# Kernel tuning notes

Measured on AMD Instinct MI355X. Metric: run time of the kernel, lower is better.

The kernel has to match this reference:

```python
import jax, jax.numpy as jnp
import numpy as np

DIM = 256
N_HEADS = 4
B, N = 2, 4096


def setup_inputs() -> dict:
    key = jax.random.key(0)
    ks = jax.random.split(key, 10)
    s = DIM ** -0.5
    return {
        "x": jax.random.normal(ks[0], (B, N, DIM), dtype=jnp.float32),
        "q_w": jax.random.normal(ks[1], (DIM, DIM), dtype=jnp.float32) * s,
        "q_b": jnp.zeros((DIM,), dtype=jnp.float32),
        "k_w": jax.random.normal(ks[2], (DIM, DIM), dtype=jnp.float32) * s,
        "k_b": jnp.zeros((DIM,), dtype=jnp.float32),
        "v_w": jax.random.normal(ks[3], (DIM, DIM), dtype=jnp.float32) * s,
        "v_b": jnp.zeros((DIM,), dtype=jnp.float32),
        "o_w": jax.random.normal(ks[4], (DIM, DIM), dtype=jnp.float32) * s,
        "o_b": jnp.zeros((DIM,), dtype=jnp.float32),
        "tau": jnp.ones((1,), dtype=jnp.float32),
    }


def reference(x, q_w, q_b, k_w, k_b, v_w, v_b, o_w, o_b, tau):
    Bsz, Nlen, C = x.shape
    H = N_HEADS
    Dh = C // H
    scale = C ** -0.5  # source uses full dim, not head_dim
    Q = (x @ q_w.T + q_b).reshape(Bsz, Nlen, H, Dh)
    K = (x @ k_w.T + k_b).reshape(Bsz, Nlen, H, Dh)
    V = (x @ v_w.T + v_b).reshape(Bsz, Nlen, H, Dh)
    attn = jnp.einsum('bnhd,bmhd->bhnm', Q, K) * scale
    # soft-threshold gate: keep only |attn| > tau, then relu
    attn = jax.nn.relu(jnp.where(jnp.abs(attn) > tau, attn, 0.0))
    attn = jax.nn.softmax(attn, axis=-1)
    out = jnp.einsum('bhnm,bmhd->bnhd', attn, V).reshape(Bsz, Nlen, C)
    return out @ o_w.T + o_b
```

## Files before the change

kernel.cpp:

```cpp
#include <hip/hip_runtime.h>

#define SEQ   4096
#define CDIM  256
#define NHEAD 4
#define DHEAD 64
#define PSTRIDE 72
#define NSPLIT 8
#define LOG2E 1.44269504f

typedef float    f32x4 __attribute__((ext_vector_type(4)));
typedef _Float16 f16x8 __attribute__((ext_vector_type(8)));
typedef _Float16 f16x4 __attribute__((ext_vector_type(4)));

__device__ __forceinline__ f16x8 cvt_frag(const float* __restrict__ p) {
    float4 f0 = *(const float4*)p;
    float4 f1 = *(const float4*)(p + 4);
    f16x8 r;
    r[0]=(_Float16)f0.x; r[1]=(_Float16)f0.y; r[2]=(_Float16)f0.z; r[3]=(_Float16)f0.w;
    r[4]=(_Float16)f1.x; r[5]=(_Float16)f1.y; r[6]=(_Float16)f1.z; r[7]=(_Float16)f1.w;
    return r;
}

__global__ __launch_bounds__(256) void sta_prep(
    const float* __restrict__ qw, const float* __restrict__ kw,
    const float* __restrict__ vw, const float* __restrict__ ow,
    _Float16* __restrict__ w16, float* __restrict__ lfull)
{
    const int mat = blockIdx.y;
    const float* src = (mat == 0) ? qw : (mat == 1) ? kw : (mat == 2) ? vw : ow;
    const int i = (blockIdx.x * 256 + threadIdx.x) * 8;
    *(f16x8*)(w16 + mat * 65536 + i) = cvt_frag(src + i);
    const int tid = (blockIdx.y * 32 + blockIdx.x) * 256 + threadIdx.x;
    lfull[tid] = 0.0f;
}

__global__ __launch_bounds__(256) void sta_qkv(
    const float* __restrict__ x, const _Float16* __restrict__ w16,
    const float* __restrict__ qb, const float* __restrict__ kb, const float* __restrict__ vb,
    _Float16* __restrict__ Qo, _Float16* __restrict__ Ko, _Float16* __restrict__ Vo)
{
    const int wave = threadIdx.x >> 6;
    const int lane = threadIdx.x & 63;
    const int l15  = lane & 15;
    const int quad = lane >> 4;
    const int mat  = blockIdx.y;
    const int half = blockIdx.z;
    const int row0 = blockIdx.x * 64 + wave * 16;

    const _Float16* w    = w16 + mat * 65536;
    const float*    bias = (mat == 0) ? qb : (mat == 1) ? kb : vb;

    f16x8 xf[8];
    const float* xrow = x + (row0 + l15) * CDIM + quad * 8;
    #pragma unroll
    for (int ks = 0; ks < 8; ks++) xf[ks] = cvt_frag(xrow + ks * 32);

    #pragma unroll 1
    for (int ct = 0; ct < 8; ct++) {
        const int ctg = half * 8 + ct;
        const _Float16* wr = w + (ctg * 16 + l15) * CDIM + quad * 8;
        f32x4 acc = {0.f, 0.f, 0.f, 0.f};
        if (mat < 2) {
            #pragma unroll
            for (int ks = 0; ks < 8; ks++)
                acc = __builtin_amdgcn_mfma_f32_16x16x32_f16(*(const f16x8*)(wr + ks * 32), xf[ks], acc, 0, 0, 0);
            const float4 bv = *(const float4*)(bias + ctg * 16 + quad * 4);
            const int c0 = ctg * 16 + quad * 4;
            const int h = c0 >> 6, d0 = c0 & 63;
            const int grow = row0 + l15, b = grow >> 12, n = grow & (SEQ - 1);
            const float sc = (mat == 0) ? (0.0625f * LOG2E) : 1.0f;
            f16x4 o;
            o[0] = (_Float16)((acc[0] + bv.x) * sc);
            o[1] = (_Float16)((acc[1] + bv.y) * sc);
            o[2] = (_Float16)((acc[2] + bv.z) * sc);
            o[3] = (_Float16)((acc[3] + bv.w) * sc);
            _Float16* dst = ((mat == 0) ? Qo : Ko) + (((b * NHEAD + h) * SEQ + n) * DHEAD + d0);
            *(f16x4*)dst = o;
        } else {
            #pragma unroll
            for (int ks = 0; ks < 8; ks++)
                acc = __builtin_amdgcn_mfma_f32_16x16x32_f16(xf[ks], *(const f16x8*)(wr + ks * 32), acc, 0, 0, 0);
            const int c = ctg * 16 + l15;
            const int h = c >> 6, d = c & 63;
            const float bv = bias[c];
            const int grow0 = row0 + quad * 4, b = grow0 >> 12, n0 = grow0 & (SEQ - 1);
            f16x4 o;
            #pragma unroll
            for (int r = 0; r < 4; r++) o[r] = (_Float16)(acc[r] + bv);
            *(f16x4*)(Vo + (((b * NHEAD + h) * DHEAD + d) * SEQ + n0)) = o;
        }
    }
}

__global__ __launch_bounds__(256) void sta_attn(
    const _Float16* __restrict__ Q, const _Float16* __restrict__ K, const _Float16* __restrict__ Vt,
    const float* __restrict__ taup,
    _Float16* __restrict__ Opart, float* __restrict__ lfull)
{
    __shared__ __align__(16) _Float16 pbuf_all[4][64 * PSTRIDE];

    const int wave = threadIdx.x >> 6;
    const int lane = threadIdx.x & 63;
    const int l15  = lane & 15;
    const int quad = lane >> 4;
    const int qt = blockIdx.x * 4 + wave;
    const int bh = blockIdx.y;
    const int sp = blockIdx.z;
    const float tau_eff = fmaxf(taup[0], 0.0f) * LOG2E;

    const _Float16* Qb = Q  + bh * SEQ * DHEAD;
    const _Float16* Kb = K  + bh * SEQ * DHEAD;
    const _Float16* Vb = Vt + bh * DHEAD * SEQ;

    const int q0 = qt * 64;
    _Float16* pbuf = pbuf_all[wave];

    f16x8 qf[4][2];
    #pragma unroll
    for (int qb = 0; qb < 4; qb++)
        #pragma unroll
        for (int ks = 0; ks < 2; ks++)
            qf[qb][ks] = *(const f16x8*)(Qb + (q0 + qb * 16 + l15) * DHEAD + ks * 32 + quad * 8);

    f32x4 O[4][4];
    #pragma unroll
    for (int qb = 0; qb < 4; qb++)
        #pragma unroll
        for (int db = 0; db < 4; db++) O[qb][db] = (f32x4){0.f, 0.f, 0.f, 0.f};
    float rs[4] = {0.f, 0.f, 0.f, 0.f};

    #pragma unroll 1
    for (int kt = sp * 8; kt < sp * 8 + 8; kt++) {
        const int kv0 = kt * 64;

        #pragma unroll
        for (int kb = 0; kb < 4; kb++) {
            const _Float16* kp = Kb + (kv0 + kb * 16 + l15) * DHEAD + quad * 8;
            f16x8 k0 = *(const f16x8*)kp;
            f16x8 k1 = *(const f16x8*)(kp + 32);
            #pragma unroll
            for (int qb = 0; qb < 4; qb++) {
                f32x4 a = {0.f, 0.f, 0.f, 0.f};
                a = __builtin_amdgcn_mfma_f32_16x16x32_f16(k0, qf[qb][0], a, 0, 0, 0);
                a = __builtin_amdgcn_mfma_f32_16x16x32_f16(k1, qf[qb][1], a, 0, 0, 0);
                f16x4 pk;
                float acc = 0.f;
                #pragma unroll
                for (int r = 0; r < 4; r++) {
                    float e = exp2f(a[r]);
                    float p = (a[r] > tau_eff) ? e : 1.0f;
                    acc += p;
                    pk[r] = (_Float16)p;
                }
                rs[qb] += acc;
                *(f16x4*)(pbuf + (qb * 16 + l15) * PSTRIDE + kb * 16 + quad * 4) = pk;
            }
        }

        #pragma unroll
        for (int ks = 0; ks < 2; ks++) {
            f16x8 pb[4];
            #pragma unroll
            for (int qb = 0; qb < 4; qb++)
                pb[qb] = *(const f16x8*)(pbuf + (qb * 16 + l15) * PSTRIDE + ks * 32 + quad * 8);
            #pragma unroll
            for (int db = 0; db < 4; db++) {
                f16x8 vf = *(const f16x8*)(Vb + (db * 16 + l15) * SEQ + kv0 + ks * 32 + quad * 8);
                #pragma unroll
                for (int qb = 0; qb < 4; qb++)
                    O[qb][db] = __builtin_amdgcn_mfma_f32_16x16x32_f16(vf, pb[qb], O[qb][db], 0, 0, 0);
            }
        }
    }

    #pragma unroll
    for (int qb = 0; qb < 4; qb++) {
        float v = rs[qb];
        v += __shfl_xor(v, 16);
        v += __shfl_xor(v, 32);
        rs[qb] = v;
    }
    _Float16* Ob = Opart + (size_t)((sp * 8 + bh) * SEQ + q0) * DHEAD;
    #pragma unroll
    for (int qb = 0; qb < 4; qb++) {
        #pragma unroll
        for (int db = 0; db < 4; db++) {
            f16x4 ov;
            #pragma unroll
            for (int r = 0; r < 4; r++) ov[r] = (_Float16)O[qb][db][r];
            *(f16x4*)(Ob + (qb * 16 + l15) * DHEAD + db * 16 + quad * 4) = ov;
        }
    }
    if (quad == 0) {
        #pragma unroll
        for (int qb = 0; qb < 4; qb++)
            atomicAdd(&lfull[bh * SEQ + q0 + qb * 16 + l15], rs[qb]);
    }
}

__global__ __launch_bounds__(128) void sta_oproj(
    const _Float16* __restrict__ Opart, const float* __restrict__ lfull,
    const _Float16* __restrict__ w16o, const float* __restrict__ ob,
    float* __restrict__ out)
{
    const int wave = threadIdx.x >> 6;
    const int lane = threadIdx.x & 63;
    const int l15  = lane & 15;
    const int quad = lane >> 4;
    const int row0 = blockIdx.x * 32 + wave * 16;
    const int quarter = blockIdx.y;

    const int grow = row0 + l15;
    const int b = grow >> 12, n = grow & (SEQ - 1);

    _Float16 inv[NHEAD];
    #pragma unroll
    for (int h = 0; h < NHEAD; h++)
        inv[h] = (_Float16)(1.0f / lfull[(b * NHEAD + h) * SEQ + n]);

    f16x8 af[8];
    #pragma unroll
    for (int ks = 0; ks < 8; ks++) {
        const int hq = ks * 4 + quad;
        const int h  = hq >> 3;
        const int d0 = (hq & 7) * 8;
        const _Float16* pp = Opart + (size_t)((b * NHEAD + h) * SEQ + n) * DHEAD + d0;
        f16x8 s = *(const f16x8*)pp;
        #pragma unroll
        for (int sp = 1; sp < NSPLIT; sp++)
            s = s + *(const f16x8*)(pp + (size_t)sp * 8 * SEQ * DHEAD);
        af[ks] = s * inv[h];
    }

    #pragma unroll 1
    for (int ct = 0; ct < 4; ct++) {
        const int ctg = quarter * 4 + ct;
        const _Float16* wr = w16o + (ctg * 16 + l15) * CDIM + quad * 8;
        f32x4 acc = {0.f, 0.f, 0.f, 0.f};
        #pragma unroll
        for (int ks = 0; ks < 8; ks++)
            acc = __builtin_amdgcn_mfma_f32_16x16x32_f16(*(const f16x8*)(wr + ks * 32), af[ks], acc, 0, 0, 0);
        const float4 bv = *(const float4*)(ob + ctg * 16 + quad * 4);
        const int c0 = ctg * 16 + quad * 4;
        float4 res;
        res.x = acc[0] + bv.x; res.y = acc[1] + bv.y;
        res.z = acc[2] + bv.z; res.w = acc[3] + bv.w;
        *(float4*)(out + (size_t)grow * CDIM + c0) = res;
    }
}

extern "C" void kernel_launch(void* const* d_in, const int* in_sizes, int n_in,
                              void* d_out, int out_size, void* d_ws, size_t ws_size,
                              hipStream_t stream) {
    const float* x   = (const float*)d_in[0];
    const float* qw  = (const float*)d_in[1];
    const float* qb  = (const float*)d_in[2];
    const float* kw  = (const float*)d_in[3];
    const float* kb  = (const float*)d_in[4];
    const float* vw  = (const float*)d_in[5];
    const float* vb  = (const float*)d_in[6];
    const float* ow  = (const float*)d_in[7];
    const float* ob  = (const float*)d_in[8];
    const float* tau = (const float*)d_in[9];

    _Float16* w16 = (_Float16*)d_ws;
    _Float16* Q   = w16 + 262144;
    _Float16* K   = Q + 2097152;
    _Float16* Vt  = K + 2097152;
    _Float16* Opart = Vt + 2097152;
    float* lfull  = (float*)(Opart + 16777216);

    sta_prep <<<dim3(32, 4),     256, 0, stream>>>(qw, kw, vw, ow, w16, lfull);
    sta_qkv  <<<dim3(128, 3, 2), 256, 0, stream>>>(x, w16, qb, kb, vb, Q, K, Vt);
    sta_attn <<<dim3(16, 8, 8),  256, 0, stream>>>(Q, K, Vt, tau, Opart, lfull);
    sta_oproj<<<dim3(256, 4),    128, 0, stream>>>(Opart, lfull, w16 + 3 * 65536, ob, (float*)d_out);
}
```

Measured before the change: 227.5 us.

## Drop weight prep kernel, double-buffer attention tiles, replace atomics with partial sums

The separate weight-conversion kernel goes away, so the QKV and output projections read fp32 weights and convert them to fp16 inline. The QKV grid loses its column-half split, so each block now covers all 16 column tiles. The attention kernel software-pipelines K loads and QK/exp against the PV step using two LDS P buffers, and asks for 2 blocks per SM via launch bounds. Row sums are stored per split and reduced in oproj instead of atomically added, which removes the zero-init. The cost is repeated fp32 weight reads and conversions, plus higher register and LDS pressure in attention.

```diff
diff --git a/kernel.cpp b/kernel.cpp
--- a/kernel.cpp
+++ b/kernel.cpp
@@ -21,22 +21,11 @@
     return r;
 }
 
-__global__ __launch_bounds__(256) void sta_prep(
-    const float* __restrict__ qw, const float* __restrict__ kw,
-    const float* __restrict__ vw, const float* __restrict__ ow,
-    _Float16* __restrict__ w16, float* __restrict__ lfull)
-{
-    const int mat = blockIdx.y;
-    const float* src = (mat == 0) ? qw : (mat == 1) ? kw : (mat == 2) ? vw : ow;
-    const int i = (blockIdx.x * 256 + threadIdx.x) * 8;
-    *(f16x8*)(w16 + mat * 65536 + i) = cvt_frag(src + i);
-    const int tid = (blockIdx.y * 32 + blockIdx.x) * 256 + threadIdx.x;
-    lfull[tid] = 0.0f;
-}
-
 __global__ __launch_bounds__(256) void sta_qkv(
-    const float* __restrict__ x, const _Float16* __restrict__ w16,
-    const float* __restrict__ qb, const float* __restrict__ kb, const float* __restrict__ vb,
+    const float* __restrict__ x,
+    const float* __restrict__ qw, const float* __restrict__ qb,
+    const float* __restrict__ kw, const float* __restrict__ kb,
+    const float* __restrict__ vw, const float* __restrict__ vb,
     _Float16* __restrict__ Qo, _Float16* __restrict__ Ko, _Float16* __restrict__ Vo)
 {
     const int wave = threadIdx.x >> 6;
@@ -44,11 +33,10 @@
     const int l15  = lane & 15;
     const int quad = lane >> 4;
     const int mat  = blockIdx.y;
-    const int half = blockIdx.z;
     const int row0 = blockIdx.x * 64 + wave * 16;
 
-    const _Float16* w    = w16 + mat * 65536;
-    const float*    bias = (mat == 0) ? qb : (mat == 1) ? kb : vb;
+    const float* w    = (mat == 0) ? qw : (mat == 1) ? kw : vw;
+    const float* bias = (mat == 0) ? qb : (mat == 1) ? kb : vb;
 
     f16x8 xf[8];
     const float* xrow = x + (row0 + l15) * CDIM + quad * 8;
@@ -56,16 +44,15 @@
     for (int ks = 0; ks < 8; ks++) xf[ks] = cvt_frag(xrow + ks * 32);
 
     #pragma unroll 1
-    for (int ct = 0; ct < 8; ct++) {
-        const int ctg = half * 8 + ct;
-        const _Float16* wr = w + (ctg * 16 + l15) * CDIM + quad * 8;
+    for (int ct = 0; ct < 16; ct++) {
+        const float* wr = w + (ct * 16 + l15) * CDIM + quad * 8;
         f32x4 acc = {0.f, 0.f, 0.f, 0.f};
         if (mat < 2) {
             #pragma unroll
             for (int ks = 0; ks < 8; ks++)
-                acc = __builtin_amdgcn_mfma_f32_16x16x32_f16(*(const f16x8*)(wr + ks * 32), xf[ks], acc, 0, 0, 0);
-            const float4 bv = *(const float4*)(bias + ctg * 16 + quad * 4);
-            const int c0 = ctg * 16 + quad * 4;
+                acc = __builtin_amdgcn_mfma_f32_16x16x32_f16(cvt_frag(wr + ks * 32), xf[ks], acc, 0, 0, 0);
+            const float4 bv = *(const float4*)(bias + ct * 16 + quad * 4);
+            const int c0 = ct * 16 + quad * 4;
             const int h = c0 >> 6, d0 = c0 & 63;
             const int grow = row0 + l15, b = grow >> 12, n = grow & (SEQ - 1);
             const float sc = (mat == 0) ? (0.0625f * LOG2E) : 1.0f;
@@ -79,8 +66,8 @@
         } else {
             #pragma unroll
             for (int ks = 0; ks < 8; ks++)
-                acc = __builtin_amdgcn_mfma_f32_16x16x32_f16(xf[ks], *(const f16x8*)(wr + ks * 32), acc, 0, 0, 0);
-            const int c = ctg * 16 + l15;
+                acc = __builtin_amdgcn_mfma_f32_16x16x32_f16(xf[ks], cvt_frag(wr + ks * 32), acc, 0, 0, 0);
+            const int c = ct * 16 + l15;
             const int h = c >> 6, d = c & 63;
             const float bv = bias[c];
             const int grow0 = row0 + quad * 4, b = grow0 >> 12, n0 = grow0 & (SEQ - 1);
@@ -92,12 +79,12 @@
     }
 }
 
-__global__ __launch_bounds__(256) void sta_attn(
+__global__ __launch_bounds__(256, 2) void sta_attn(
     const _Float16* __restrict__ Q, const _Float16* __restrict__ K, const _Float16* __restrict__ Vt,
     const float* __restrict__ taup,
-    _Float16* __restrict__ Opart, float* __restrict__ lfull)
+    _Float16* __restrict__ Opart, float* __restrict__ lpart)
 {
-    __shared__ __align__(16) _Float16 pbuf_all[4][64 * PSTRIDE];
+    __shared__ __align__(16) _Float16 pbuf_all[4][2][64 * PSTRIDE];
 
     const int wave = threadIdx.x >> 6;
     const int lane = threadIdx.x & 63;
@@ -113,7 +100,6 @@
     const _Float16* Vb = Vt + bh * DHEAD * SEQ;
 
     const int q0 = qt * 64;
-    _Float16* pbuf = pbuf_all[wave];
 
     f16x8 qf[4][2];
     #pragma unroll
@@ -129,20 +115,28 @@
         for (int db = 0; db < 4; db++) O[qb][db] = (f32x4){0.f, 0.f, 0.f, 0.f};
     float rs[4] = {0.f, 0.f, 0.f, 0.f};
 
-    #pragma unroll 1
-    for (int kt = sp * 8; kt < sp * 8 + 8; kt++) {
+    f16x8 kfA[8], kfB[8];
+    _Float16* buf0 = pbuf_all[wave][0];
+    _Float16* buf1 = pbuf_all[wave][1];
+    const int first = sp * 8;
+
+    auto loadK = [&](int kt, f16x8* kf) {
         const int kv0 = kt * 64;
-
         #pragma unroll
         for (int kb = 0; kb < 4; kb++) {
             const _Float16* kp = Kb + (kv0 + kb * 16 + l15) * DHEAD + quad * 8;
-            f16x8 k0 = *(const f16x8*)kp;
-            f16x8 k1 = *(const f16x8*)(kp + 32);
+            kf[2 * kb]     = *(const f16x8*)kp;
+            kf[2 * kb + 1] = *(const f16x8*)(kp + 32);
+        }
+    };
+    auto qkexp = [&](const f16x8* kf, _Float16* pb) {
+        #pragma unroll
+        for (int kb = 0; kb < 4; kb++) {
             #pragma unroll
             for (int qb = 0; qb < 4; qb++) {
                 f32x4 a = {0.f, 0.f, 0.f, 0.f};
-                a = __builtin_amdgcn_mfma_f32_16x16x32_f16(k0, qf[qb][0], a, 0, 0, 0);
-                a = __builtin_amdgcn_mfma_f32_16x16x32_f16(k1, qf[qb][1], a, 0, 0, 0);
+                a = __builtin_amdgcn_mfma_f32_16x16x32_f16(kf[2 * kb],     qf[qb][0], a, 0, 0, 0);
+                a = __builtin_amdgcn_mfma_f32_16x16x32_f16(kf[2 * kb + 1], qf[qb][1], a, 0, 0, 0);
                 f16x4 pk;
                 float acc = 0.f;
                 #pragma unroll
@@ -153,25 +147,44 @@
                     pk[r] = (_Float16)p;
                 }
                 rs[qb] += acc;
-                *(f16x4*)(pbuf + (qb * 16 + l15) * PSTRIDE + kb * 16 + quad * 4) = pk;
+                *(f16x4*)(pb + (qb * 16 + l15) * PSTRIDE + kb * 16 + quad * 4) = pk;
             }
         }
-
+    };
+    auto pv = [&](int kt, const _Float16* pb) {
+        const int kv0 = kt * 64;
         #pragma unroll
         for (int ks = 0; ks < 2; ks++) {
-            f16x8 pb[4];
+            f16x8 pfr[4];
             #pragma unroll
             for (int qb = 0; qb < 4; qb++)
-                pb[qb] = *(const f16x8*)(pbuf + (qb * 16 + l15) * PSTRIDE + ks * 32 + quad * 8);
+                pfr[qb] = *(const f16x8*)(pb + (qb * 16 + l15) * PSTRIDE + ks * 32 + quad * 8);
             #pragma unroll
             for (int db = 0; db < 4; db++) {
                 f16x8 vf = *(const f16x8*)(Vb + (db * 16 + l15) * SEQ + kv0 + ks * 32 + quad * 8);
                 #pragma unroll
                 for (int qb = 0; qb < 4; qb++)
-                    O[qb][db] = __builtin_amdgcn_mfma_f32_16x16x32_f16(vf, pb[qb], O[qb][db], 0, 0, 0);
+                    O[qb][db] = __builtin_amdgcn_mfma_f32_16x16x32_f16(vf, pfr[qb], O[qb][db], 0, 0, 0);
             }
         }
-    }
+    };
+
+    loadK(first, kfA);
+    qkexp(kfA, buf0);
+    #pragma unroll 1
+    for (int i = 0; i < 3; i++) {
+        const int kt = first + 2 * i;
+        loadK(kt + 1, kfB);
+        pv(kt, buf0);
+        qkexp(kfB, buf1);
+        loadK(kt + 2, kfA);
+        pv(kt + 1, buf1);
+        qkexp(kfA, buf0);
+    }
+    loadK(first + 7, kfB);
+    pv(first + 6, buf0);
+    qkexp(kfB, buf1);
+    pv(first + 7, buf1);
 
     #pragma unroll
     for (int qb = 0; qb < 4; qb++) {
@@ -194,13 +207,13 @@
     if (quad == 0) {
         #pragma unroll
         for (int qb = 0; qb < 4; qb++)
-            atomicAdd(&lfull[bh * SEQ + q0 + qb * 16 + l15], rs[qb]);
+            lpart[(sp * 8 + bh) * SEQ + q0 + qb * 16 + l15] = rs[qb];
     }
 }
 
 __global__ __launch_bounds__(128) void sta_oproj(
-    const _Float16* __restrict__ Opart, const float* __restrict__ lfull,
-    const _Float16* __restrict__ w16o, const float* __restrict__ ob,
+    const _Float16* __restrict__ Opart, const float* __restrict__ lpart,
+    const float* __restrict__ ow, const float* __restrict__ ob,
     float* __restrict__ out)
 {
     const int wave = threadIdx.x >> 6;
@@ -215,8 +228,13 @@
 
     _Float16 inv[NHEAD];
     #pragma unroll
-    for (int h = 0; h < NHEAD; h++)
-        inv[h] = (_Float16)(1.0f / lfull[(b * NHEAD + h) * SEQ + n]);
+    for (int h = 0; h < NHEAD; h++) {
+        float l = 0.f;
+        #pragma unroll
+        for (int sp = 0; sp < NSPLIT; sp++)
+            l += lpart[(sp * 8 + b * NHEAD + h) * SEQ + n];
+        inv[h] = (_Float16)(1.0f / l);
+    }
 
     f16x8 af[8];
     #pragma unroll
@@ -235,11 +253,11 @@
     #pragma unroll 1
     for (int ct = 0; ct < 4; ct++) {
         const int ctg = quarter * 4 + ct;
-        const _Float16* wr = w16o + (ctg * 16 + l15) * CDIM + quad * 8;
+        const float* wr = ow + (ctg * 16 + l15) * CDIM + quad * 8;
         f32x4 acc = {0.f, 0.f, 0.f, 0.f};
         #pragma unroll
         for (int ks = 0; ks < 8; ks++)
-            acc = __builtin_amdgcn_mfma_f32_16x16x32_f16(*(const f16x8*)(wr + ks * 32), af[ks], acc, 0, 0, 0);
+            acc = __builtin_amdgcn_mfma_f32_16x16x32_f16(cvt_frag(wr + ks * 32), af[ks], acc, 0, 0, 0);
         const float4 bv = *(const float4*)(ob + ctg * 16 + quad * 4);
         const int c0 = ctg * 16 + quad * 4;
         float4 res;
@@ -263,15 +281,13 @@
     const float* ob  = (const float*)d_in[8];
     const float* tau = (const float*)d_in[9];
 
-    _Float16* w16 = (_Float16*)d_ws;
-    _Float16* Q   = w16 + 262144;
+    _Float16* Q   = (_Float16*)d_ws;
     _Float16* K   = Q + 2097152;
     _Float16* Vt  = K + 2097152;
     _Float16* Opart = Vt + 2097152;
-    float* lfull  = (float*)(Opart + 16777216);
-
-    sta_prep <<<dim3(32, 4),     256, 0, stream>>>(qw, kw, vw, ow, w16, lfull);
-    sta_qkv  <<<dim3(128, 3, 2), 256, 0, stream>>>(x, w16, qb, kb, vb, Q, K, Vt);
-    sta_attn <<<dim3(16, 8, 8),  256, 0, stream>>>(Q, K, Vt, tau, Opart, lfull);
-    sta_oproj<<<dim3(256, 4),    128, 0, stream>>>(Opart, lfull, w16 + 3 * 65536, ob, (float*)d_out);
-}
+    float* lpart  = (float*)(Opart + 16777216);
+
+    sta_qkv  <<<dim3(128, 3), 256, 0, stream>>>(x, qw, qb, kw, kb, vw, vb, Q, K, Vt);
+    sta_attn <<<dim3(16, 8, 8), 256, 0, stream>>>(Q, K, Vt, tau, Opart, lpart);
+    sta_oproj<<<dim3(256, 4), 128, 0, stream>>>(Opart, lpart, ow, ob, (float*)d_out);
+}
```

New measurement: 290.0 us. 27.5% more time.
